# Kernel tuning notes

Hardware: AMD Instinct MI355X
Metric: run time of the kernel (lower is better)

Reference implementation:

```python
import jax, jax.numpy as jnp
import numpy as np

B, M, RPI = 16, 80, 256            # images, objects/image, relations/image
N, R = B * M, B * RPI
DF, REP, EMB, HID, NH, L = 12544, 1024, 256, 512, 8, 4
OBJC, RELC = 151, 51
IMW, IMH = 800.0, 600.0


def _ln(x, g, b):
    m = x.mean(-1, keepdims=True)
    v = ((x - m) ** 2).mean(-1, keepdims=True)
    return (x - m) * jax.lax.rsqrt(v + 1e-5) * g + b


def _encoder(x, qkv_w, qkv_b, out_w, out_b, f1_w, f1_b, f2_w, f2_b, ln1_s, ln1_b, ln2_s, ln2_b):
    # post-LN transformer encoder, L layers, x: [B, M, HID]
    Bb, Mm, D = x.shape
    dk = D // NH
    scale = 1.0 / jnp.sqrt(jnp.float32(dk))
    for l in range(L):
        qkv = x @ qkv_w[l].T + qkv_b[l]
        q, k, v = jnp.split(qkv, 3, axis=-1)
        hs = lambda t: t.reshape(Bb, Mm, NH, dk).transpose(0, 2, 1, 3)
        q, k, v = hs(q), hs(k), hs(v)
        att = jax.nn.softmax(jnp.einsum('bhqd,bhkd->bhqk', q, k) * scale, axis=-1)
        o = jnp.einsum('bhqk,bhkd->bhqd', att, v).transpose(0, 2, 1, 3).reshape(Bb, Mm, D)
        x = _ln(x + o @ out_w[l].T + out_b[l], ln1_s[l], ln1_b[l])
        f = jax.nn.relu(x @ f1_w[l].T + f1_b[l]) @ f2_w[l].T + f2_b[l]
        x = _ln(x + f, ln2_s[l], ln2_b[l])
    return x


def _box_info(boxes):
    wh = boxes[:, 2:] - boxes[:, :2] + 1.0
    xy = boxes[:, :2] + 0.5 * wh
    w, h = wh[:, :1], wh[:, 1:]
    x, y = xy[:, :1], xy[:, 1:]
    x1, y1, x2, y2 = boxes[:, 0:1], boxes[:, 1:2], boxes[:, 2:3], boxes[:, 3:4]
    return jnp.concatenate([w / IMW, h / IMH, x / IMW, y / IMH, x1 / IMW, y1 / IMH,
                            x2 / IMW, y2 / IMH, w * h / (IMW * IMH)], axis=-1)  # [N, 9]


def setup_inputs() -> dict:
    key = jax.random.key(0)
    ks = iter(jax.random.split(key, 80))
    nrm = lambda shape, s=0.02: jax.random.normal(next(ks), shape, jnp.float32) * s
    d = {}
    d['features'] = jax.random.normal(next(ks), (N, DF), jnp.float32)
    d['union_features'] = jax.random.normal(next(ks), (R, REP), jnp.float32)
    x1 = jax.random.uniform(next(ks), (N, 1)) * (IMW - 120.0)
    y1 = jax.random.uniform(next(ks), (N, 1)) * (IMH - 120.0)
    w = jax.random.uniform(next(ks), (N, 1)) * 100.0 + 5.0
    h = jax.random.uniform(next(ks), (N, 1)) * 100.0 + 5.0
    d['boxes'] = jnp.concatenate([x1, y1, x1 + w, y1 + h], axis=-1)
    d['logits'] = jax.random.normal(next(ks), (N, OBJC), jnp.float32)
    d['labels'] = jax.random.randint(next(ks), (N,), 0, OBJC)
    d['rel_pair_idxs'] = jax.random.randint(next(ks), (B, RPI, 2), 0, M)
    # feature extractor
    d['fe1_w'] = nrm((REP, DF)); d['fe1_b'] = jnp.zeros((REP,))
    d['fe2_w'] = nrm((REP, REP)); d['fe2_b'] = jnp.zeros((REP,))
    # embeddings
    d['emb1'] = nrm((OBJC, EMB), 1.0)
    d['emb2'] = nrm((OBJC, EMB), 1.0)
    # bbox embed 9->32->128
    d['bb1_w'] = nrm((32, 9)); d['bb1_b'] = jnp.zeros((32,))
    d['bb2_w'] = nrm((128, 32)); d['bb2_b'] = jnp.zeros((128,))
    d['lobj_w'] = nrm((HID, REP + EMB + 128)); d['lobj_b'] = jnp.zeros((HID,))
    d['ledge_w'] = nrm((HID, EMB + HID)); d['ledge_b'] = jnp.zeros((HID,))
    for p in ('o', 'e'):
        d[p + 'qkv_w'] = nrm((L, 3 * HID, HID)); d[p + 'qkv_b'] = jnp.zeros((L, 3 * HID))
        d[p + 'out_w'] = nrm((L, HID, HID)); d[p + 'out_b'] = jnp.zeros((L, HID))
        d[p + 'f1_w'] = nrm((L, HID, HID)); d[p + 'f1_b'] = jnp.zeros((L, HID))
        d[p + 'f2_w'] = nrm((L, HID, HID)); d[p + 'f2_b'] = jnp.zeros((L, HID))
        d[p + 'ln1_s'] = jnp.ones((L, HID)); d[p + 'ln1_b'] = jnp.zeros((L, HID))
        d[p + 'ln2_s'] = jnp.ones((L, HID)); d[p + 'ln2_b'] = jnp.zeros((L, HID))
    d['pcat_w'] = nrm((REP, 2 * HID)); d['pcat_b'] = jnp.zeros((REP,))
    d['fuse_w'] = nrm((REP, REP + HID)); d['fuse_b'] = jnp.zeros((REP,))
    d['cpx_w'] = nrm((RELC, 2 * REP)); d['cpx_b'] = jnp.zeros((RELC,))
    d['dpath_w'] = nrm((RELC, REP)); d['dpath_b'] = jnp.zeros((RELC,))
    return d


def reference(features, union_features, boxes, logits,
              fe1_w, fe1_b, fe2_w, fe2_b, emb1, emb2,
              bb1_w, bb1_b, bb2_w, bb2_b, lobj_w, lobj_b, ledge_w, ledge_b,
              oqkv_w, oqkv_b, oout_w, oout_b, of1_w, of1_b, of2_w, of2_b,
              oln1_s, oln1_b, oln2_s, oln2_b,
              eqkv_w, eqkv_b, eout_w, eout_b, ef1_w, ef1_b, ef2_w, ef2_b,
              eln1_s, eln1_b, eln2_s, eln2_b,
              pcat_w, pcat_b, fuse_w, fuse_b, cpx_w, cpx_b, dpath_w, dpath_b,
              labels, rel_pair_idxs):
    # FeatureExtractor
    bf = jax.nn.relu(features @ fe1_w.T + fe1_b)
    bf = jax.nn.relu(bf @ fe2_w.T + fe2_b)                        # [N, REP]
    # bbox embedding (dropout = identity in eval)
    pos = jax.nn.relu(_box_info(boxes) @ bb1_w.T + bb1_b)
    pos = jax.nn.relu(pos @ bb2_w.T + bb2_b)                      # [N, 128]
    obj_rep = jnp.concatenate([bf, emb1[labels], pos], -1) @ lobj_w.T + lobj_b  # [N, HID]
    obj_emb = _encoder(obj_rep.reshape(B, M, HID), oqkv_w, oqkv_b, oout_w, oout_b,
                       of1_w, of1_b, of2_w, of2_b, oln1_s, oln1_b, oln2_s, oln2_b)  # [B, M, HID]
    edge_in = jnp.concatenate([obj_emb.reshape(N, HID), emb2[labels]], -1) @ ledge_w.T + ledge_b
    gctx = _encoder(edge_in.reshape(B, M, HID), eqkv_w, eqkv_b, eout_w, eout_b,
                    ef1_w, ef1_b, ef2_w, ef2_b, eln1_s, eln1_b, eln2_s, eln2_b).mean(axis=1)  # [B, HID]
    # pair gather per image
    head = jax.vmap(lambda e, i: e[i])(obj_emb, rel_pair_idxs[:, :, 0])  # [B, RPI, HID]
    tail = jax.vmap(lambda e, i: e[i])(obj_emb, rel_pair_idxs[:, :, 1])
    pair = jnp.concatenate([head, tail], -1).reshape(R, 2 * HID)
    local = pair @ pcat_w.T + pcat_b                               # [R, REP]
    gexp = jnp.repeat(gctx, RPI, axis=0)                           # [R, HID]
    sem = jax.nn.relu(jnp.concatenate([local, gexp], -1) @ fuse_w.T + fuse_b)
    final = jnp.concatenate([sem, union_features], -1)             # [R, 2*REP]
    rel_logits = final @ cpx_w.T + cpx_b + local @ dpath_w.T + dpath_b  # [R, RELC]
    return rel_logits
```

## Files before the change

kernel.cpp:

```cpp
#include <hip/hip_runtime.h>
#include <hip/hip_bf16.h>
#include <cstdint>

#define DEV_INLINE __device__ __forceinline__

using u16 = unsigned short;
typedef __attribute__((ext_vector_type(8))) short bf8_t;
typedef __attribute__((ext_vector_type(4))) float f32x4;

constexpr int cB = 16, cM = 80, cRPI = 256;
constexpr int cN = cB * cM;
constexpr int cR = cB * cRPI;
constexpr int cDF = 12544, cREP = 1024, cEMB = 256, cHID = 512, cNH = 8, cL = 4;
constexpr int cRELC = 51;

DEV_INLINE u16 f2bf(float x) { return __builtin_bit_cast(u16, __float2bfloat16(x)); }
DEV_INLINE float bf2f(u16 u) { return __bfloat162float(__builtin_bit_cast(__hip_bfloat16, u)); }

DEV_INLINE float wave_max(float v) {
#pragma unroll
  for (int o = 32; o; o >>= 1) v = fmaxf(v, __shfl_xor(v, o));
  return v;
}
DEV_INLINE float wave_sum(float v) {
#pragma unroll
  for (int o = 32; o; o >>= 1) v += __shfl_xor(v, o);
  return v;
}

DEV_INLINE void xcd_remap(int& bx, int& by) {
  const int gx = gridDim.x;
  const int nwg = gx * gridDim.y;
  const int id = blockIdx.x + gx * blockIdx.y;
  const int q = nwg >> 3, r = nwg & 7;
  const int x = id & 7, k = id >> 3;
  const int idp = (x < r) ? x * (q + 1) + k : r * (q + 1) + (x - r) * q + k;
  bx = idp % gx;
  by = idp / gx;
}

template <int BM, int BN, bool SPLIT>
__global__ __launch_bounds__(256) void gemm_h(
    const u16* __restrict__ A, int lda,
    const u16* __restrict__ Bw, int ldb,
    int Mr, int Nr, int Klen,
    float* __restrict__ outF, int ldc,
    u16* __restrict__ outH, int ldh,
    const float* __restrict__ bias,
    const float* __restrict__ res, int resld, int resmode,
    int relu)
{
  constexpr int MF = BM / 32, NF = BN / 32;
  __shared__ u16 As[2][BM * 32];
  __shared__ u16 Bs[2][BN * 32];
  const int tid = threadIdx.x;
  const int wid = tid >> 6, lane = tid & 63;
  const int l15 = lane & 15, l4 = lane >> 4;
  int bx, by;
  xcd_remap(bx, by);
  const int bm = by * BM, bn = bx * BN;
  const int wr = wid >> 1, wc = wid & 1;
  const int kbase = SPLIT ? blockIdx.z * Klen : 0;

  f32x4 acc[MF][NF] = {};

  constexpr int AISS = (BM * 4) / 256;
  constexpr int BISS = (BN * 4) / 256;

  auto stage = [&](int buf, int ks) {
    const int k0 = kbase + (ks << 5);
#pragma unroll
    for (int i = 0; i < AISS; ++i) {
      const int c = i * 256 + tid;
      const int row = c >> 2, seg = c & 3;
      const int sseg = seg ^ (row & 3);
      const u16* gp = A + (size_t)(bm + row) * lda + k0 + sseg * 8;
      __builtin_amdgcn_global_load_lds(
          (const __attribute__((address_space(1))) void*)gp,
          (__attribute__((address_space(3))) void*)((char*)As[buf] + (size_t)(i * 256 + wid * 64) * 16),
          16, 0, 0);
    }
#pragma unroll
    for (int i = 0; i < BISS; ++i) {
      const int c = i * 256 + tid;
      const int row = c >> 2, seg = c & 3;
      const int sseg = seg ^ (row & 3);
      int brow = bn + row; if (brow > Nr - 1) brow = Nr - 1;
      const u16* gp = Bw + (size_t)brow * ldb + k0 + sseg * 8;
      __builtin_amdgcn_global_load_lds(
          (const __attribute__((address_space(1))) void*)gp,
          (__attribute__((address_space(3))) void*)((char*)Bs[buf] + (size_t)(i * 256 + wid * 64) * 16),
          16, 0, 0);
    }
  };

  const int nk = Klen >> 5;
  stage(0, 0);
  __syncthreads();

  for (int ks = 0; ks < nk; ++ks) {
    const int cur = ks & 1;
    if (ks + 1 < nk) stage(cur ^ 1, ks + 1);

    bf8_t af[MF], bfr[NF];
#pragma unroll
    for (int m = 0; m < MF; ++m) {
      const int r = wr * (BM / 2) + m * 16 + l15;
      const int g = l4 ^ (r & 3);
      af[m] = *(const bf8_t*)&As[cur][r * 32 + g * 8];
    }
#pragma unroll
    for (int n = 0; n < NF; ++n) {
      const int r = wc * (BN / 2) + n * 16 + l15;
      const int g = l4 ^ (r & 3);
      bfr[n] = *(const bf8_t*)&Bs[cur][r * 32 + g * 8];
    }
#pragma unroll
    for (int m = 0; m < MF; ++m)
#pragma unroll
      for (int n = 0; n < NF; ++n)
        acc[m][n] = __builtin_amdgcn_mfma_f32_16x16x32_bf16(af[m], bfr[n], acc[m][n], 0, 0, 0);
    __syncthreads();
  }

  if (SPLIT) {
    float* po = outF + (size_t)blockIdx.z * Mr * ldc;
#pragma unroll
    for (int m = 0; m < MF; ++m)
#pragma unroll
      for (int n = 0; n < NF; ++n) {
        const int ccol = bn + wc * (BN / 2) + n * 16 + l15;
        if (ccol >= Nr) continue;
#pragma unroll
        for (int g = 0; g < 4; ++g) {
          const int r = bm + wr * (BM / 2) + m * 16 + l4 * 4 + g;
          po[(size_t)r * ldc + ccol] = acc[m][n][g];
        }
      }
  } else {
#pragma unroll
    for (int m = 0; m < MF; ++m)
#pragma unroll
      for (int n = 0; n < NF; ++n) {
        const int ccol = bn + wc * (BN / 2) + n * 16 + l15;
        if (ccol >= Nr) continue;
        const float bv = bias ? bias[ccol] : 0.f;
#pragma unroll
        for (int g = 0; g < 4; ++g) {
          const int r = bm + wr * (BM / 2) + m * 16 + l4 * 4 + g;
          float v = acc[m][n][g] + bv;
          if (resmode == 1) v += res[(size_t)r * resld + ccol];
          else if (resmode == 2) v += res[(size_t)(r >> 8) * resld + ccol];
          if (relu) v = fmaxf(v, 0.f);
          if (outF) outF[(size_t)r * ldc + ccol] = v;
          if (outH) outH[(size_t)r * ldh + ccol] = f2bf(v);
        }
      }
  }
}

template <int BM, int BN>
static void g16(hipStream_t s, const u16* A, int lda, const u16* W, int ldb,
                int M, int N, int K, float* outF, int ldc, u16* outH, int ldh,
                const float* bias, const float* res, int resld, int resmode, int relu) {
  dim3 g((N + BN - 1) / BN, M / BM);
  gemm_h<BM, BN, false><<<g, 256, 0, s>>>(A, lda, W, ldb, M, N, K, outF, ldc, outH, ldh,
                                          bias, res, resld, resmode, relu);
}

__global__ __launch_bounds__(256) void gemm_nt(
    const float* __restrict__ A, int lda,
    const float* __restrict__ Bw, int ldb,
    float* __restrict__ C, int ldc,
    const float* __restrict__ bias,
    int Mr, int Nr, int Kr, int flags)
{
  __shared__ float As[16][68];
  __shared__ float Bs[16][68];
  const int tid = threadIdx.x;
  const int tx = tid & 15, ty = tid >> 4;
  const int bm = blockIdx.y * 64, bn = blockIdx.x * 64;
  const int lr = tid >> 2;
  const int lk = (tid & 3) * 4;

  float acc[4][4];
#pragma unroll
  for (int i = 0; i < 4; ++i)
#pragma unroll
    for (int j = 0; j < 4; ++j) acc[i][j] = 0.f;

  for (int k0 = 0; k0 < Kr; k0 += 16) {
    const int ar = bm + lr, br = bn + lr;
#pragma unroll
    for (int j = 0; j < 4; ++j) {
      const int kk = k0 + lk + j;
      float va = 0.f, vb = 0.f;
      if (kk < Kr) {
        if (ar < Mr) va = A[(size_t)ar * lda + kk];
        if (br < Nr) vb = Bw[(size_t)br * ldb + kk];
      }
      As[lk + j][lr] = va;
      Bs[lk + j][lr] = vb;
    }
    __syncthreads();
#pragma unroll
    for (int kk = 0; kk < 16; ++kk) {
      const float a0 = As[kk][ty * 4 + 0], a1 = As[kk][ty * 4 + 1],
                  a2 = As[kk][ty * 4 + 2], a3 = As[kk][ty * 4 + 3];
      const float b0 = Bs[kk][tx * 4 + 0], b1 = Bs[kk][tx * 4 + 1],
                  b2 = Bs[kk][tx * 4 + 2], b3 = Bs[kk][tx * 4 + 3];
      acc[0][0] += a0 * b0; acc[0][1] += a0 * b1; acc[0][2] += a0 * b2; acc[0][3] += a0 * b3;
      acc[1][0] += a1 * b0; acc[1][1] += a1 * b1; acc[1][2] += a1 * b2; acc[1][3] += a1 * b3;
      acc[2][0] += a2 * b0; acc[2][1] += a2 * b1; acc[2][2] += a2 * b2; acc[2][3] += a2 * b3;
      acc[3][0] += a3 * b0; acc[3][1] += a3 * b1; acc[3][2] += a3 * b2; acc[3][3] += a3 * b3;
    }
    __syncthreads();
  }
#pragma unroll
  for (int i = 0; i < 4; ++i) {
    const int r = bm + ty * 4 + i;
    if (r >= Mr) continue;
#pragma unroll
    for (int j = 0; j < 4; ++j) {
      const int c = bn + tx * 4 + j;
      if (c >= Nr) continue;
      float v = acc[i][j];
      if (bias) v += bias[c];
      if (flags & 2) v = fmaxf(v, 0.f);
      C[(size_t)r * ldc + c] = v;
    }
  }
}

__global__ void conv_kernel(const float* __restrict__ s, u16* __restrict__ d, int n4) {
  const int i = blockIdx.x * 256 + threadIdx.x;
  if (i >= n4) return;
  const float4 v = ((const float4*)s)[i];
  ushort4 o;
  o.x = f2bf(v.x); o.y = f2bf(v.y); o.z = f2bf(v.z); o.w = f2bf(v.w);
  ((ushort4*)d)[i] = o;
}

__global__ void conv2d_kernel(const float* __restrict__ src, int slda,
                              u16* __restrict__ dst, int dld, int cols) {
  const int r = blockIdx.x;
  for (int c = threadIdx.x; c < cols; c += blockDim.x)
    dst[(size_t)r * dld + c] = f2bf(src[(size_t)r * slda + c]);
}

__global__ void addb_kernel(const float* a, const float* b, float* o, int n) {
  const int i = threadIdx.x;
  if (i < n) o[i] = a[i] + b[i];
}

__global__ void box_info_kernel(const float* __restrict__ boxes, float* __restrict__ bi) {
  const int i = blockIdx.x * blockDim.x + threadIdx.x;
  if (i >= cN) return;
  const float x1 = boxes[i * 4 + 0], y1 = boxes[i * 4 + 1];
  const float x2 = boxes[i * 4 + 2], y2 = boxes[i * 4 + 3];
  const float w = x2 - x1 + 1.f, h = y2 - y1 + 1.f;
  const float cx = x1 + 0.5f * w, cy = y1 + 0.5f * h;
  float* o = bi + (size_t)i * 9;
  o[0] = w / 800.f;  o[1] = h / 600.f;
  o[2] = cx / 800.f; o[3] = cy / 600.f;
  o[4] = x1 / 800.f; o[5] = y1 / 600.f;
  o[6] = x2 / 800.f; o[7] = y2 / 600.f;
  o[8] = (w * h) / (800.f * 600.f);
}

__global__ void gather_emb_h(const float* __restrict__ emb, const int* __restrict__ labels,
                             u16* __restrict__ dst, int dld) {
  const int i = blockIdx.x;
  const int l = labels[i];
  const float* s = emb + (size_t)l * cEMB;
  for (int c = threadIdx.x; c < cEMB; c += blockDim.x)
    dst[(size_t)i * dld + c] = f2bf(s[c]);
}

__global__ __launch_bounds__(256) void attn_kernel(const u16* __restrict__ qkv,
                                                   u16* __restrict__ o) {
  __shared__ float Ks[80][65];
  __shared__ float Vs[80][65];
  const int bh = blockIdx.x;
  const int b = bh >> 3, h = bh & 7;
  const int tid = threadIdx.x;
  const u16* base = qkv + (size_t)(b * cM) * 1536 + h * 64;

  for (int e = tid; e < 80 * 64; e += 256) {
    const int r = e >> 6, d = e & 63;
    Ks[r][d] = bf2f(base[(size_t)r * 1536 + 512 + d]);
    Vs[r][d] = bf2f(base[(size_t)r * 1536 + 1024 + d]);
  }
  __syncthreads();

  const int wave = tid >> 6, lane = tid & 63;
  const int r0 = blockIdx.y * 16;
  for (int r = r0 + wave; r < r0 + 16; r += 4) {
    const float qd = bf2f(base[(size_t)r * 1536 + lane]);
    const int c2 = 64 + lane;
    const int c2c = (c2 < 80) ? c2 : 0;
    float s0 = 0.f, s1 = 0.f;
#pragma unroll 8
    for (int d = 0; d < 64; ++d) {
      const float qv = __shfl(qd, d);
      s0 += qv * Ks[lane][d];
      s1 += qv * Ks[c2c][d];
    }
    s0 *= 0.125f;
    s1 = (c2 < 80) ? s1 * 0.125f : -1e30f;
    const float mx = wave_max(fmaxf(s0, s1));
    const float p0 = __expf(s0 - mx);
    const float p1 = (c2 < 80) ? __expf(s1 - mx) : 0.f;
    const float ssum = wave_sum(p0 + p1);

    float od = 0.f;
#pragma unroll 8
    for (int c = 0; c < 64; ++c) od += __shfl(p0, c) * Vs[c][lane];
#pragma unroll
    for (int c = 0; c < 16; ++c) od += __shfl(p1, c) * Vs[64 + c][lane];
    od /= ssum;
    o[(size_t)(b * cM + r) * cHID + h * 64 + lane] = f2bf(od);
  }
}

__global__ __launch_bounds__(256) void ln_kernel(
    const float* __restrict__ in, float* __restrict__ outF,
    u16* __restrict__ outH, int ldh,
    const float* __restrict__ g, const float* __restrict__ bta) {
  const int row = blockIdx.x * 4 + (threadIdx.x >> 6);
  const int lane = threadIdx.x & 63;
  const float* x = in + (size_t)row * cHID;
  float v[8];
  float s = 0.f;
#pragma unroll
  for (int i = 0; i < 8; ++i) { v[i] = x[lane + i * 64]; s += v[i]; }
  s = wave_sum(s);
  const float mean = s * (1.f / 512.f);
  float vs = 0.f;
#pragma unroll
  for (int i = 0; i < 8; ++i) { const float d = v[i] - mean; vs += d * d; }
  vs = wave_sum(vs);
  const float inv = rsqrtf(vs * (1.f / 512.f) + 1e-5f);
#pragma unroll
  for (int i = 0; i < 8; ++i) {
    const int c = lane + i * 64;
    const float y = (v[i] - mean) * inv * g[c] + bta[c];
    outF[(size_t)row * cHID + c] = y;
    outH[(size_t)row * ldh + c] = f2bf(y);
  }
}

__global__ void mean_kernel(const float* __restrict__ x, float* __restrict__ gctx) {
  const int b = blockIdx.x;
  const int c = threadIdx.x;
  float s = 0.f;
  for (int m = 0; m < cM; ++m) s += x[(size_t)(b * cM + m) * cHID + c];
  gctx[(size_t)b * cHID + c] = s * (1.f / 80.f);
}

__global__ void pair_gather_h(const u16* __restrict__ obj, int old, const int* __restrict__ idx,
                              u16* __restrict__ pair) {
  const int r = blockIdx.x;
  const int b = r >> 8, rr = r & 255;
  const int i0 = idx[(size_t)(b * cRPI + rr) * 2 + 0];
  const int i1 = idx[(size_t)(b * cRPI + rr) * 2 + 1];
  const u16* hsrc = obj + (size_t)(b * cM + i0) * old;
  const u16* tsrc = obj + (size_t)(b * cM + i1) * old;
  u16* p = pair + (size_t)r * 1024;
  for (int c = threadIdx.x; c < cHID; c += blockDim.x) {
    p[c] = hsrc[c];
    p[cHID + c] = tsrc[c];
  }
}

__global__ void reduce8_kernel(const float* __restrict__ p, const float* __restrict__ bias,
                               u16* __restrict__ outH) {
  const int idx = blockIdx.x * 256 + threadIdx.x;
  constexpr int total = cN * cREP;
  if (idx >= total) return;
  float v = bias[idx & 1023];
#pragma unroll
  for (int z = 0; z < 8; ++z) v += p[(size_t)z * total + idx];
  outH[idx] = f2bf(fmaxf(v, 0.f));
}

__global__ void freduce_kernel(const float* __restrict__ p, const float* __restrict__ biasc,
                               float* __restrict__ out) {
  const int idx = blockIdx.x * 256 + threadIdx.x;
  if (idx >= cR * cRELC) return;
  const int r = idx / cRELC, c = idx - r * cRELC;
  float v = biasc[c];
#pragma unroll
  for (int z = 0; z < 4; ++z) v += p[(size_t)z * cR * 64 + (size_t)r * 64 + c];
  out[idx] = v;
}

static void run_encoder(hipStream_t s, float* x, u16* xh, u16* qkvh, u16* attn_h,
                        float* res1, u16* f_h,
                        const u16* qkvw, const float* qkvb,
                        const u16* outw, const float* outb,
                        const u16* f1w, const float* f1b,
                        const u16* f2w, const float* f2b,
                        const float* ln1s, const float* ln1b,
                        const float* ln2s, const float* ln2b,
                        u16* last_bf, int last_ld) {
  for (int l = 0; l < cL; ++l) {
    g16<64, 64>(s, xh, 512, qkvw + (size_t)l * 1536 * 512, 512, cN, 1536, 512,
                nullptr, 0, qkvh, 1536, qkvb + l * 1536, nullptr, 0, 0, 0);
    attn_kernel<<<dim3(cB * cNH, 5), 256, 0, s>>>(qkvh, attn_h);
    g16<64, 64>(s, attn_h, 512, outw + (size_t)l * 512 * 512, 512, cN, 512, 512,
                res1, 512, nullptr, 0, outb + l * 512, x, 512, 1, 0);
    ln_kernel<<<cN / 4, 256, 0, s>>>(res1, x, xh, 512, ln1s + l * 512, ln1b + l * 512);
    g16<64, 64>(s, xh, 512, f1w + (size_t)l * 512 * 512, 512, cN, 512, 512,
                nullptr, 0, f_h, 512, f1b + l * 512, nullptr, 0, 0, 1);
    g16<64, 64>(s, f_h, 512, f2w + (size_t)l * 512 * 512, 512, cN, 512, 512,
                res1, 512, nullptr, 0, f2b + l * 512, x, 512, 1, 0);
    const bool last = (l == cL - 1);
    ln_kernel<<<cN / 4, 256, 0, s>>>(res1, x, last ? last_bf : xh, last ? last_ld : 512,
                                     ln2s + l * 512, ln2b + l * 512);
  }
}

constexpr size_t OFF_FEAT  = 0;
constexpr size_t OFF_FE1W  = 32112640;
constexpr size_t OFF_PART  = 57802752;
constexpr size_t P_END     = 99745792;
constexpr size_t OFF_PAIR  = 0;
constexpr size_t OFF_FINAL = 8388608;
constexpr size_t OFF_OBJIN = 33554432;
constexpr size_t OFF_QKVH  = 37158912;
constexpr size_t OFF_X     = 41091072;
constexpr size_t OFF_XH    = 43712512;
constexpr size_t OFF_ATTN  = 45023232;
constexpr size_t OFF_RES   = 46333952;
constexpr size_t OFF_FH    = 48955392;
constexpr size_t OFF_EDGE  = 50266112;

extern "C" void kernel_launch(void* const* d_in, const int* in_sizes, int n_in,
                              void* d_out, int out_size, void* d_ws, size_t ws_size,
                              hipStream_t stream) {
  (void)in_sizes; (void)n_in; (void)out_size; (void)ws_size;

  const float* features = (const float*)d_in[0];
  const float* unionf   = (const float*)d_in[1];
  const float* boxes    = (const float*)d_in[2];
  const int*   labels   = (const int*)d_in[4];
  const int*   relidx   = (const int*)d_in[5];
  const float* fe1_w = (const float*)d_in[6];
  const float* fe1_b = (const float*)d_in[7];
  const float* fe2_w = (const float*)d_in[8];
  const float* fe2_b = (const float*)d_in[9];
  const float* emb1  = (const float*)d_in[10];
  const float* emb2  = (const float*)d_in[11];
  const float* bb1_w = (const float*)d_in[12];
  const float* bb1_b = (const float*)d_in[13];
  const float* bb2_w = (const float*)d_in[14];
  const float* bb2_b = (const float*)d_in[15];
  const float* lobj_w = (const float*)d_in[16];
  const float* lobj_b = (const float*)d_in[17];
  const float* ledge_w = (const float*)d_in[18];
  const float* ledge_b = (const float*)d_in[19];
  const float* oqkv_w = (const float*)d_in[20];
  const float* oqkv_b = (const float*)d_in[21];
  const float* oout_w = (const float*)d_in[22];
  const float* oout_b = (const float*)d_in[23];
  const float* of1_w = (const float*)d_in[24];
  const float* of1_b = (const float*)d_in[25];
  const float* of2_w = (const float*)d_in[26];
  const float* of2_b = (const float*)d_in[27];
  const float* oln1_s = (const float*)d_in[28];
  const float* oln1_b = (const float*)d_in[29];
  const float* oln2_s = (const float*)d_in[30];
  const float* oln2_b = (const float*)d_in[31];
  const float* eqkv_w = (const float*)d_in[32];
  const float* eqkv_b = (const float*)d_in[33];
  const float* eout_w = (const float*)d_in[34];
  const float* eout_b = (const float*)d_in[35];
  const float* ef1_w = (const float*)d_in[36];
  const float* ef1_b = (const float*)d_in[37];
  const float* ef2_w = (const float*)d_in[38];
  const float* ef2_b = (const float*)d_in[39];
  const float* eln1_s = (const float*)d_in[40];
  const float* eln1_b = (const float*)d_in[41];
  const float* eln2_s = (const float*)d_in[42];
  const float* eln2_b = (const float*)d_in[43];
  const float* pcat_w = (const float*)d_in[44];
  const float* pcat_b = (const float*)d_in[45];
  const float* fuse_w = (const float*)d_in[46];
  const float* fuse_b = (const float*)d_in[47];
  const float* cpx_w  = (const float*)d_in[48];
  const float* cpx_b  = (const float*)d_in[49];
  const float* dpath_w = (const float*)d_in[50];
  const float* dpath_b = (const float*)d_in[51];

  char* wsb = (char*)d_ws;
  u16* feat_h  = (u16*)(wsb + OFF_FEAT);
  u16* fe1w_h  = (u16*)(wsb + OFF_FE1W);
  float* part  = (float*)(wsb + OFF_PART);
  u16* pair    = (u16*)(wsb + OFF_PAIR);
  u16* finalb  = (u16*)(wsb + OFF_FINAL);
  u16* obj_in  = (u16*)(wsb + OFF_OBJIN);
  u16* qkvh    = (u16*)(wsb + OFF_QKVH);
  float* x     = (float*)(wsb + OFF_X);
  u16* xh      = (u16*)(wsb + OFF_XH);
  u16* attn_h  = (u16*)(wsb + OFF_ATTN);
  float* res1  = (float*)(wsb + OFF_RES);
  u16* f_h     = (u16*)(wsb + OFF_FH);
  u16* edge_in = (u16*)(wsb + OFF_EDGE);

  size_t off = P_END;
  auto alloc = [&](size_t bytes) { char* p = wsb + off; off = (off + bytes + 255) & ~(size_t)255; return p; };
  u16* fe2w_h   = (u16*)alloc(2097152);
  u16* lobjw_h  = (u16*)alloc(1441792);
  u16* ledgew_h = (u16*)alloc(786432);
  u16* oqkvw_h  = (u16*)alloc(6291456);
  u16* ooutw_h  = (u16*)alloc(2097152);
  u16* of1w_h   = (u16*)alloc(2097152);
  u16* of2w_h   = (u16*)alloc(2097152);
  u16* eqkvw_h  = (u16*)alloc(6291456);
  u16* eoutw_h  = (u16*)alloc(2097152);
  u16* ef1w_h   = (u16*)alloc(2097152);
  u16* ef2w_h   = (u16*)alloc(2097152);
  u16* pcatw_h  = (u16*)alloc(2097152);
  u16* fusew_h  = (u16*)alloc(3145728);
  u16* catw     = (u16*)alloc(313344);
  float* biasc  = (float*)alloc(256);
  u16* bf0h     = (u16*)alloc(2621440);
  float* gctx   = (float*)alloc(131072);
  u16* gctx_h   = (u16*)alloc(65536);
  float* gcproj = (float*)alloc(262144);
  float* binfo  = (float*)alloc(46080);
  float* pos1   = (float*)alloc(163840);
  float* pos2   = (float*)alloc(655360);
  float* fpart  = (float*)alloc(4194304);

  auto conv = [&](const float* s, u16* d, size_t n) {
    const int n4 = (int)(n / 4);
    conv_kernel<<<(n4 + 255) / 256, 256, 0, stream>>>(s, d, n4);
  };

  conv(features, feat_h, (size_t)cN * cDF);
  conv(fe1_w, fe1w_h, (size_t)cREP * cDF);
  conv(fe2_w, fe2w_h, (size_t)cREP * cREP);
  conv(lobj_w, lobjw_h, (size_t)cHID * 1408);
  conv(ledge_w, ledgew_h, (size_t)cHID * 768);
  conv(oqkv_w, oqkvw_h, (size_t)cL * 1536 * 512);
  conv(oout_w, ooutw_h, (size_t)cL * 512 * 512);
  conv(of1_w, of1w_h, (size_t)cL * 512 * 512);
  conv(of2_w, of2w_h, (size_t)cL * 512 * 512);
  conv(eqkv_w, eqkvw_h, (size_t)cL * 1536 * 512);
  conv(eout_w, eoutw_h, (size_t)cL * 512 * 512);
  conv(ef1_w, ef1w_h, (size_t)cL * 512 * 512);
  conv(ef2_w, ef2w_h, (size_t)cL * 512 * 512);
  conv(pcat_w, pcatw_h, (size_t)cREP * 1024);
  conv(fuse_w, fusew_h, (size_t)cREP * 1536);
  conv2d_kernel<<<cRELC, 256, 0, stream>>>(cpx_w, 2048, catw, 3072, 2048);
  conv2d_kernel<<<cRELC, 256, 0, stream>>>(dpath_w, 1024, catw + 2048, 3072, 1024);
  addb_kernel<<<1, 64, 0, stream>>>(cpx_b, dpath_b, biasc, cRELC);

  gemm_h<128, 128, true><<<dim3(8, 10, 8), 256, 0, stream>>>(
      feat_h, cDF, fe1w_h, cDF, cN, cREP, cDF / 8, part, cREP,
      nullptr, 0, nullptr, nullptr, 0, 0, 0);
  reduce8_kernel<<<(cN * cREP + 255) / 256, 256, 0, stream>>>(part, fe1_b, bf0h);

  box_info_kernel<<<(cN + 255) / 256, 256, 0, stream>>>(boxes, binfo);
  gemm_nt<<<dim3(1, 20), 256, 0, stream>>>(binfo, 9, bb1_w, 9, pos1, 32, bb1_b, cN, 32, 9, 2);
  gemm_nt<<<dim3(2, 20), 256, 0, stream>>>(pos1, 32, bb2_w, 32, pos2, 128, bb2_b, cN, 128, 32, 2);
  conv2d_kernel<<<cN, 128, 0, stream>>>(pos2, 128, obj_in + 1280, 1408, 128);
  gather_emb_h<<<cN, 256, 0, stream>>>(emb1, labels, obj_in + 1024, 1408);

  g16<64, 64>(stream, bf0h, 1024, fe2w_h, 1024, cN, cREP, cREP,
              nullptr, 0, obj_in, 1408, fe2_b, nullptr, 0, 0, 1);

  g16<64, 64>(stream, obj_in, 1408, lobjw_h, 1408, cN, cHID, 1408,
              x, 512, xh, 512, lobj_b, nullptr, 0, 0, 0);

  run_encoder(stream, x, xh, qkvh, attn_h, res1, f_h,
              oqkvw_h, oqkv_b, ooutw_h, oout_b, of1w_h, of1_b, of2w_h, of2_b,
              oln1_s, oln1_b, oln2_s, oln2_b, edge_in, 768);

  gather_emb_h<<<cN, 256, 0, stream>>>(emb2, labels, edge_in + 512, 768);
  pair_gather_h<<<cR, 256, 0, stream>>>(edge_in, 768, relidx, pair);

  g16<64, 64>(stream, edge_in, 768, ledgew_h, 768, cN, cHID, 768,
              x, 512, xh, 512, ledge_b, nullptr, 0, 0, 0);
  run_encoder(stream, x, xh, qkvh, attn_h, res1, f_h,
              eqkvw_h, eqkv_b, eoutw_h, eout_b, ef1w_h, ef1_b, ef2w_h, ef2_b,
              eln1_s, eln1_b, eln2_s, eln2_b, xh, 512);
  mean_kernel<<<cB, cHID, 0, stream>>>(x, gctx);

  conv2d_kernel<<<16, 256, 0, stream>>>(gctx, 512, gctx_h, 512, 512);
  g16<64, 64>(stream, gctx_h, 512, fusew_h + 1024, 1536, 64, cREP, 512,
              gcproj, 1024, nullptr, 0, fuse_b, nullptr, 0, 0, 0);

  conv2d_kernel<<<cR, 256, 0, stream>>>(unionf, 1024, finalb + 1024, 3072, 1024);
  g16<128, 64>(stream, pair, 1024, pcatw_h, 1024, cR, cREP, 1024,
               nullptr, 0, finalb + 2048, 3072, pcat_b, nullptr, 0, 0, 0);
  g16<128, 64>(stream, finalb + 2048, 3072, fusew_h, 1536, cR, cREP, 1024,
               nullptr, 0, finalb, 3072, nullptr, gcproj, 1024, 2, 1);

  gemm_h<64, 64, true><<<dim3(1, 64, 4), 256, 0, stream>>>(
      finalb, 3072, catw, 3072, cR, cRELC, 3072 / 4, fpart, 64,
      nullptr, 0, nullptr, nullptr, 0, 0, 0);
  freduce_kernel<<<(cR * cRELC + 255) / 256, 256, 0, stream>>>(fpart, biasc, (float*)d_out);
}
```

Baseline: 1.008 ms.

## Fuse LayerNorm into encoder GEMMs, batch conversions, merge box MLP prep

Adds a GEMM kernel that applies LayerNorm to the residual rows, stages the normalized bf16 row block in LDS, and then runs the QKV or FFN1 projection on it. This removes separate ln_kernel launches and round trips inside the encoder loop. It also merges the many per-weight fp32→bf16 conversion launches into a few grid-stride kernels, fuses the box-info, two small MLP layers and embedding gather into one prep kernel, and shrinks most GEMM tiles to 32x64 to get more blocks. The trade-off is that each column block recomputes the LayerNorm for its rows, and the smaller tiles give less data reuse per block.

```diff
diff --git a/kernel.cpp b/kernel.cpp
--- a/kernel.cpp
+++ b/kernel.cpp
@@ -50,7 +50,8 @@
     const float* __restrict__ res, int resld, int resmode,
     int relu)
 {
-  constexpr int MF = BM / 32, NF = BN / 32;
+  constexpr int MF = BM > 32 ? BM / 32 : 1, NF = BN > 32 ? BN / 32 : 1;
+  constexpr int ACH = BM * 4, BCH = BN * 4;
   __shared__ u16 As[2][BM * 32];
   __shared__ u16 Bs[2][BN * 32];
   const int tid = threadIdx.x;
@@ -64,33 +65,34 @@
 
   f32x4 acc[MF][NF] = {};
 
-  constexpr int AISS = (BM * 4) / 256;
-  constexpr int BISS = (BN * 4) / 256;
-
   auto stage = [&](int buf, int ks) {
     const int k0 = kbase + (ks << 5);
 #pragma unroll
-    for (int i = 0; i < AISS; ++i) {
+    for (int i = 0; i < (ACH + 255) / 256; ++i) {
       const int c = i * 256 + tid;
-      const int row = c >> 2, seg = c & 3;
-      const int sseg = seg ^ (row & 3);
-      const u16* gp = A + (size_t)(bm + row) * lda + k0 + sseg * 8;
-      __builtin_amdgcn_global_load_lds(
-          (const __attribute__((address_space(1))) void*)gp,
-          (__attribute__((address_space(3))) void*)((char*)As[buf] + (size_t)(i * 256 + wid * 64) * 16),
-          16, 0, 0);
-    }
-#pragma unroll
-    for (int i = 0; i < BISS; ++i) {
+      if (ACH % 256 == 0 || c < ACH) {
+        const int row = c >> 2, seg = c & 3;
+        const int sseg = seg ^ (row & 3);
+        const u16* gp = A + (size_t)(bm + row) * lda + k0 + sseg * 8;
+        __builtin_amdgcn_global_load_lds(
+            (const __attribute__((address_space(1))) void*)gp,
+            (__attribute__((address_space(3))) void*)((char*)As[buf] + (size_t)(i * 256 + wid * 64) * 16),
+            16, 0, 0);
+      }
+    }
+#pragma unroll
+    for (int i = 0; i < (BCH + 255) / 256; ++i) {
       const int c = i * 256 + tid;
-      const int row = c >> 2, seg = c & 3;
-      const int sseg = seg ^ (row & 3);
-      int brow = bn + row; if (brow > Nr - 1) brow = Nr - 1;
-      const u16* gp = Bw + (size_t)brow * ldb + k0 + sseg * 8;
-      __builtin_amdgcn_global_load_lds(
-          (const __attribute__((address_space(1))) void*)gp,
-          (__attribute__((address_space(3))) void*)((char*)Bs[buf] + (size_t)(i * 256 + wid * 64) * 16),
-          16, 0, 0);
+      if (BCH % 256 == 0 || c < BCH) {
+        const int row = c >> 2, seg = c & 3;
+        const int sseg = seg ^ (row & 3);
+        int brow = bn + row; if (brow > Nr - 1) brow = Nr - 1;
+        const u16* gp = Bw + (size_t)brow * ldb + k0 + sseg * 8;
+        __builtin_amdgcn_global_load_lds(
+            (const __attribute__((address_space(1))) void*)gp,
+            (__attribute__((address_space(3))) void*)((char*)Bs[buf] + (size_t)(i * 256 + wid * 64) * 16),
+            16, 0, 0);
+      }
     }
   };
 
@@ -168,77 +170,182 @@
                                           bias, res, resld, resmode, relu);
 }
 
-__global__ __launch_bounds__(256) void gemm_nt(
-    const float* __restrict__ A, int lda,
-    const float* __restrict__ Bw, int ldb,
-    float* __restrict__ C, int ldc,
-    const float* __restrict__ bias,
-    int Mr, int Nr, int Kr, int flags)
+__global__ __launch_bounds__(256) void gemm_lnA(
+    const float* __restrict__ res,
+    const float* __restrict__ lnS, const float* __restrict__ lnB,
+    const u16* __restrict__ W, int Nr,
+    u16* __restrict__ outH, int ldh,
+    const float* __restrict__ bias, int relu,
+    float* __restrict__ xout)
 {
-  __shared__ float As[16][68];
-  __shared__ float Bs[16][68];
+  __shared__ u16 As[32 * 512];
+  __shared__ u16 Bs[2][64 * 32];
   const int tid = threadIdx.x;
-  const int tx = tid & 15, ty = tid >> 4;
-  const int bm = blockIdx.y * 64, bn = blockIdx.x * 64;
-  const int lr = tid >> 2;
-  const int lk = (tid & 3) * 4;
-
-  float acc[4][4];
-#pragma unroll
-  for (int i = 0; i < 4; ++i)
-#pragma unroll
-    for (int j = 0; j < 4; ++j) acc[i][j] = 0.f;
-
-  for (int k0 = 0; k0 < Kr; k0 += 16) {
-    const int ar = bm + lr, br = bn + lr;
-#pragma unroll
-    for (int j = 0; j < 4; ++j) {
-      const int kk = k0 + lk + j;
-      float va = 0.f, vb = 0.f;
-      if (kk < Kr) {
-        if (ar < Mr) va = A[(size_t)ar * lda + kk];
-        if (br < Nr) vb = Bw[(size_t)br * ldb + kk];
-      }
-      As[lk + j][lr] = va;
-      Bs[lk + j][lr] = vb;
+  const int wid = tid >> 6, lane = tid & 63;
+  const int l15 = lane & 15, l4 = lane >> 4;
+  int bx, by;
+  xcd_remap(bx, by);
+  const int bm = by * 32, bn = bx * 64;
+  const int wr = wid >> 1, wc = wid & 1;
+
+  const int r8 = tid >> 3, sub = tid & 7;
+  const float4* rp4 = (const float4*)(res + (size_t)(bm + r8) * 512 + sub * 64);
+  float s = 0.f, q = 0.f;
+#pragma unroll
+  for (int k = 0; k < 16; ++k) {
+    const float4 v = rp4[k];
+    s += v.x + v.y + v.z + v.w;
+    q += v.x * v.x + v.y * v.y + v.z * v.z + v.w * v.w;
+  }
+#pragma unroll
+  for (int m = 1; m < 8; m <<= 1) { s += __shfl_xor(s, m); q += __shfl_xor(q, m); }
+  const float mean = s * (1.f / 512.f);
+  const float inv = rsqrtf(q * (1.f / 512.f) - mean * mean + 1e-5f);
+  const float4* ls4 = (const float4*)(lnS + sub * 64);
+  const float4* lb4 = (const float4*)(lnB + sub * 64);
+  float4* xo4 = (xout && bx == 0)
+      ? (float4*)(xout + (size_t)(bm + r8) * 512 + sub * 64) : nullptr;
+#pragma unroll
+  for (int k2 = 0; k2 < 8; ++k2) {
+    const float4 a = rp4[k2 * 2], b = rp4[k2 * 2 + 1];
+    const float4 sa = ls4[k2 * 2], sb = ls4[k2 * 2 + 1];
+    const float4 ba = lb4[k2 * 2], bb = lb4[k2 * 2 + 1];
+    float y0 = (a.x - mean) * inv * sa.x + ba.x;
+    float y1 = (a.y - mean) * inv * sa.y + ba.y;
+    float y2 = (a.z - mean) * inv * sa.z + ba.z;
+    float y3 = (a.w - mean) * inv * sa.w + ba.w;
+    float y4 = (b.x - mean) * inv * sb.x + bb.x;
+    float y5 = (b.y - mean) * inv * sb.y + bb.y;
+    float y6 = (b.z - mean) * inv * sb.z + bb.z;
+    float y7 = (b.w - mean) * inv * sb.w + bb.w;
+    bf8_t wv;
+    wv[0] = (short)f2bf(y0); wv[1] = (short)f2bf(y1);
+    wv[2] = (short)f2bf(y2); wv[3] = (short)f2bf(y3);
+    wv[4] = (short)f2bf(y4); wv[5] = (short)f2bf(y5);
+    wv[6] = (short)f2bf(y6); wv[7] = (short)f2bf(y7);
+    const int gsw = ((sub << 3) | k2) ^ (r8 & 7);
+    *(bf8_t*)&As[r8 * 512 + gsw * 8] = wv;
+    if (xo4) {
+      xo4[k2 * 2] = make_float4(y0, y1, y2, y3);
+      xo4[k2 * 2 + 1] = make_float4(y4, y5, y6, y7);
+    }
+  }
+
+  auto stageW = [&](int buf, int ks) {
+    const int row = tid >> 2, seg = tid & 3;
+    const int sseg = seg ^ (row & 3);
+    int brow = bn + row; if (brow > Nr - 1) brow = Nr - 1;
+    const u16* gp = W + (size_t)brow * 512 + (ks << 5) + sseg * 8;
+    __builtin_amdgcn_global_load_lds(
+        (const __attribute__((address_space(1))) void*)gp,
+        (__attribute__((address_space(3))) void*)((char*)Bs[buf] + (size_t)(wid * 64) * 16),
+        16, 0, 0);
+  };
+
+  stageW(0, 0);
+  __syncthreads();
+
+  f32x4 acc[2] = {};
+  for (int ks = 0; ks < 16; ++ks) {
+    const int cur = ks & 1;
+    if (ks + 1 < 16) stageW(cur ^ 1, ks + 1);
+
+    const int ra = wr * 16 + l15;
+    const int ga = ((ks << 2) | l4) ^ (ra & 7);
+    const bf8_t af = *(const bf8_t*)&As[ra * 512 + ga * 8];
+#pragma unroll
+    for (int n = 0; n < 2; ++n) {
+      const int rb = wc * 32 + n * 16 + l15;
+      const int gb = l4 ^ (rb & 3);
+      const bf8_t bv = *(const bf8_t*)&Bs[cur][rb * 32 + gb * 8];
+      acc[n] = __builtin_amdgcn_mfma_f32_16x16x32_bf16(af, bv, acc[n], 0, 0, 0);
     }
     __syncthreads();
-#pragma unroll
-    for (int kk = 0; kk < 16; ++kk) {
-      const float a0 = As[kk][ty * 4 + 0], a1 = As[kk][ty * 4 + 1],
-                  a2 = As[kk][ty * 4 + 2], a3 = As[kk][ty * 4 + 3];
-      const float b0 = Bs[kk][tx * 4 + 0], b1 = Bs[kk][tx * 4 + 1],
-                  b2 = Bs[kk][tx * 4 + 2], b3 = Bs[kk][tx * 4 + 3];
-      acc[0][0] += a0 * b0; acc[0][1] += a0 * b1; acc[0][2] += a0 * b2; acc[0][3] += a0 * b3;
-      acc[1][0] += a1 * b0; acc[1][1] += a1 * b1; acc[1][2] += a1 * b2; acc[1][3] += a1 * b3;
-      acc[2][0] += a2 * b0; acc[2][1] += a2 * b1; acc[2][2] += a2 * b2; acc[2][3] += a2 * b3;
-      acc[3][0] += a3 * b0; acc[3][1] += a3 * b1; acc[3][2] += a3 * b2; acc[3][3] += a3 * b3;
-    }
-    __syncthreads();
-  }
-#pragma unroll
-  for (int i = 0; i < 4; ++i) {
-    const int r = bm + ty * 4 + i;
-    if (r >= Mr) continue;
-#pragma unroll
-    for (int j = 0; j < 4; ++j) {
-      const int c = bn + tx * 4 + j;
-      if (c >= Nr) continue;
-      float v = acc[i][j];
-      if (bias) v += bias[c];
-      if (flags & 2) v = fmaxf(v, 0.f);
-      C[(size_t)r * ldc + c] = v;
-    }
-  }
-}
-
-__global__ void conv_kernel(const float* __restrict__ s, u16* __restrict__ d, int n4) {
-  const int i = blockIdx.x * 256 + threadIdx.x;
-  if (i >= n4) return;
-  const float4 v = ((const float4*)s)[i];
-  ushort4 o;
-  o.x = f2bf(v.x); o.y = f2bf(v.y); o.z = f2bf(v.z); o.w = f2bf(v.w);
-  ((ushort4*)d)[i] = o;
+  }
+
+#pragma unroll
+  for (int n = 0; n < 2; ++n) {
+    const int col = bn + wc * 32 + n * 16 + l15;
+    if (col >= Nr) continue;
+    const float bv = bias[col];
+#pragma unroll
+    for (int g = 0; g < 4; ++g) {
+      const int r = bm + wr * 16 + l4 * 4 + g;
+      float v = acc[n][g] + bv;
+      if (relu) v = fmaxf(v, 0.f);
+      outH[(size_t)r * ldh + col] = f2bf(v);
+    }
+  }
+}
+
+__global__ void conv_big2(const float* __restrict__ f, const float* __restrict__ w,
+                          u16* __restrict__ fh, u16* __restrict__ wh) {
+  constexpr int N1 = cN * cDF / 4;
+  constexpr int N2 = cREP * cDF / 4;
+  for (int i = blockIdx.x * 256 + threadIdx.x; i < N1 + N2; i += gridDim.x * 256) {
+    const float4 v = (i < N1) ? ((const float4*)f)[i] : ((const float4*)w)[i - N1];
+    ushort4 o = {f2bf(v.x), f2bf(v.y), f2bf(v.z), f2bf(v.w)};
+    if (i < N1) ((ushort4*)fh)[i] = o; else ((ushort4*)wh)[i - N1] = o;
+  }
+}
+
+constexpr size_t W_FE2 = 0, W_LOBJ = W_FE2 + 1048576, W_LEDGE = W_LOBJ + 720896,
+  W_OQKV = W_LEDGE + 393216, W_OOUT = W_OQKV + 3145728, W_OF1 = W_OOUT + 1048576,
+  W_OF2 = W_OF1 + 1048576, W_EQKV = W_OF2 + 1048576, W_EOUT = W_EQKV + 3145728,
+  W_EF1 = W_EOUT + 1048576, W_EF2 = W_EF1 + 1048576, W_PCAT = W_EF2 + 1048576,
+  W_FUSE = W_PCAT + 1048576, W_WEND = W_FUSE + 1572864;
+
+struct EncSrcs {
+  const float *fe2, *lobj, *ledge, *oqkv, *oout, *of1, *of2,
+              *eqkv, *eout, *ef1, *ef2, *pcat, *fuse;
+};
+
+__global__ void conv_enc(EncSrcs S, u16* __restrict__ wb) {
+#define SEG(nm, OFF, PRE, LEN) \
+  if (i < (PRE) + (LEN)) { \
+    const float4 v = ((const float4*)S.nm)[i - (PRE)]; \
+    ushort4 o = {f2bf(v.x), f2bf(v.y), f2bf(v.z), f2bf(v.w)}; \
+    ((ushort4*)(wb + (OFF)))[i - (PRE)] = o; \
+  } else
+  for (int i = blockIdx.x * 256 + threadIdx.x; i < (int)(W_WEND / 4); i += gridDim.x * 256) {
+    SEG(fe2,  W_FE2,   0,       262144)
+    SEG(lobj, W_LOBJ,  262144,  180224)
+    SEG(ledge,W_LEDGE, 442368,  98304)
+    SEG(oqkv, W_OQKV,  540672,  786432)
+    SEG(oout, W_OOUT,  1327104, 262144)
+    SEG(of1,  W_OF1,   1589248, 262144)
+    SEG(of2,  W_OF2,   1851392, 262144)
+    SEG(eqkv, W_EQKV,  2113536, 786432)
+    SEG(eout, W_EOUT,  2899968, 262144)
+    SEG(ef1,  W_EF1,   3162112, 262144)
+    SEG(ef2,  W_EF2,   3424256, 262144)
+    SEG(pcat, W_PCAT,  3686400, 262144)
+    SEG(fuse, W_FUSE,  3948544, 393216)
+    { }
+  }
+#undef SEG
+}
+
+__global__ void conv_cat(const float* __restrict__ cpx, const float* __restrict__ dpath,
+                         const float* __restrict__ cb, const float* __restrict__ db,
+                         u16* __restrict__ catw, float* __restrict__ biasc) {
+  constexpr int N1 = cRELC * 512;
+  constexpr int N2 = cRELC * 256;
+  const int i0 = blockIdx.x * 256 + threadIdx.x;
+  if (blockIdx.x == 0 && threadIdx.x < cRELC) biasc[threadIdx.x] = cb[threadIdx.x] + db[threadIdx.x];
+  for (int i = i0; i < N1 + N2; i += gridDim.x * 256) {
+    if (i < N1) {
+      const int r = i >> 9, c = i & 511;
+      const float4 v = ((const float4*)cpx)[i];
+      ushort4 o = {f2bf(v.x), f2bf(v.y), f2bf(v.z), f2bf(v.w)};
+      ((ushort4*)catw)[r * 768 + c] = o;
+    } else {
+      const int j = i - N1, r = j >> 8, c = j & 255;
+      const float4 v = ((const float4*)dpath)[j];
+      ushort4 o = {f2bf(v.x), f2bf(v.y), f2bf(v.z), f2bf(v.w)};
+      ((ushort4*)catw)[r * 768 + 512 + c] = o;
+    }
+  }
 }
 
 __global__ void conv2d_kernel(const float* __restrict__ src, int slda,
@@ -248,24 +355,43 @@
     dst[(size_t)r * dld + c] = f2bf(src[(size_t)r * slda + c]);
 }
 
-__global__ void addb_kernel(const float* a, const float* b, float* o, int n) {
-  const int i = threadIdx.x;
-  if (i < n) o[i] = a[i] + b[i];
-}
-
-__global__ void box_info_kernel(const float* __restrict__ boxes, float* __restrict__ bi) {
-  const int i = blockIdx.x * blockDim.x + threadIdx.x;
-  if (i >= cN) return;
-  const float x1 = boxes[i * 4 + 0], y1 = boxes[i * 4 + 1];
-  const float x2 = boxes[i * 4 + 2], y2 = boxes[i * 4 + 3];
+__global__ __launch_bounds__(256) void prep_obj(
+    const float* __restrict__ boxes,
+    const float* __restrict__ bb1w, const float* __restrict__ bb1b,
+    const float* __restrict__ bb2w, const float* __restrict__ bb2b,
+    const float* __restrict__ emb1, const int* __restrict__ labels,
+    u16* __restrict__ obj_in) {
+  __shared__ float W1[288];
+  __shared__ float W2[4096];
+  __shared__ float P1[8][33];
+  const int tid = threadIdx.x;
+  for (int i = tid; i < 288; i += 256) W1[i] = bb1w[i];
+  for (int i = tid; i < 4096; i += 256) W2[i] = bb2w[i];
+  __syncthreads();
+  const int r8 = tid >> 5, sub = tid & 31;
+  const int row = blockIdx.x * 8 + r8;
+  const float x1 = boxes[row * 4], y1 = boxes[row * 4 + 1];
+  const float x2 = boxes[row * 4 + 2], y2 = boxes[row * 4 + 3];
   const float w = x2 - x1 + 1.f, h = y2 - y1 + 1.f;
-  const float cx = x1 + 0.5f * w, cy = y1 + 0.5f * h;
-  float* o = bi + (size_t)i * 9;
-  o[0] = w / 800.f;  o[1] = h / 600.f;
-  o[2] = cx / 800.f; o[3] = cy / 600.f;
-  o[4] = x1 / 800.f; o[5] = y1 / 600.f;
-  o[6] = x2 / 800.f; o[7] = y2 / 600.f;
-  o[8] = (w * h) / (800.f * 600.f);
+  const float bi[9] = {w / 800.f, h / 600.f, (x1 + 0.5f * w) / 800.f, (y1 + 0.5f * h) / 600.f,
+                       x1 / 800.f, y1 / 600.f, x2 / 800.f, y2 / 600.f, w * h / 480000.f};
+  float p = bb1b[sub];
+#pragma unroll
+  for (int j = 0; j < 9; ++j) p += bi[j] * W1[sub * 9 + j];
+  P1[r8][sub] = fmaxf(p, 0.f);
+  __syncthreads();
+#pragma unroll
+  for (int jo = 0; jo < 4; ++jo) {
+    const int o = sub + jo * 32;
+    float a = bb2b[o];
+#pragma unroll
+    for (int j2 = 0; j2 < 32; ++j2) a += P1[r8][j2] * W2[o * 32 + j2];
+    obj_in[(size_t)row * 1408 + 1280 + o] = f2bf(fmaxf(a, 0.f));
+  }
+  const int l = labels[row];
+#pragma unroll
+  for (int k = 0; k < 8; ++k)
+    obj_in[(size_t)row * 1408 + 1024 + sub + k * 32] = f2bf(emb1[(size_t)l * 256 + sub + k * 32]);
 }
 
 __global__ void gather_emb_h(const float* __restrict__ emb, const int* __restrict__ labels,
@@ -350,12 +476,12 @@
   }
 }
 
-__global__ void mean_kernel(const float* __restrict__ x, float* __restrict__ gctx) {
+__global__ void mean_kernel(const float* __restrict__ x, u16* __restrict__ gctx_h) {
   const int b = blockIdx.x;
   const int c = threadIdx.x;
   float s = 0.f;
   for (int m = 0; m < cM; ++m) s += x[(size_t)(b * cM + m) * cHID + c];
-  gctx[(size_t)b * cHID + c] = s * (1.f / 80.f);
+  gctx_h[(size_t)b * cHID + c] = f2bf(s * (1.f / 80.f));
 }
 
 __global__ void pair_gather_h(const u16* __restrict__ obj, int old, const int* __restrict__ idx,
@@ -395,8 +521,8 @@
   out[idx] = v;
 }
 
-static void run_encoder(hipStream_t s, float* x, u16* xh, u16* qkvh, u16* attn_h,
-                        float* res1, u16* f_h,
+static void run_encoder(hipStream_t s, float* x, float* xa, float* res1,
+                        u16* xh, u16* qkvh, u16* attn_h, u16* f_h,
                         const u16* qkvw, const float* qkvb,
                         const u16* outw, const float* outb,
                         const u16* f1w, const float* f1b,
@@ -405,20 +531,26 @@
                         const float* ln2s, const float* ln2b,
                         u16* last_bf, int last_ld) {
   for (int l = 0; l < cL; ++l) {
-    g16<64, 64>(s, xh, 512, qkvw + (size_t)l * 1536 * 512, 512, cN, 1536, 512,
-                nullptr, 0, qkvh, 1536, qkvb + l * 1536, nullptr, 0, 0, 0);
+    if (l == 0) {
+      g16<32, 64>(s, xh, 512, qkvw, 512, cN, 1536, 512,
+                  nullptr, 0, qkvh, 1536, qkvb, nullptr, 0, 0, 0);
+    } else {
+      gemm_lnA<<<dim3(24, cN / 32), 256, 0, s>>>(
+          res1, ln2s + (l - 1) * 512, ln2b + (l - 1) * 512,
+          qkvw + (size_t)l * 1536 * 512, 1536, qkvh, 1536,
+          qkvb + l * 1536, 0, x);
+    }
     attn_kernel<<<dim3(cB * cNH, 5), 256, 0, s>>>(qkvh, attn_h);
-    g16<64, 64>(s, attn_h, 512, outw + (size_t)l * 512 * 512, 512, cN, 512, 512,
+    g16<32, 64>(s, attn_h, 512, outw + (size_t)l * 512 * 512, 512, cN, 512, 512,
                 res1, 512, nullptr, 0, outb + l * 512, x, 512, 1, 0);
-    ln_kernel<<<cN / 4, 256, 0, s>>>(res1, x, xh, 512, ln1s + l * 512, ln1b + l * 512);
-    g16<64, 64>(s, xh, 512, f1w + (size_t)l * 512 * 512, 512, cN, 512, 512,
-                nullptr, 0, f_h, 512, f1b + l * 512, nullptr, 0, 0, 1);
-    g16<64, 64>(s, f_h, 512, f2w + (size_t)l * 512 * 512, 512, cN, 512, 512,
-                res1, 512, nullptr, 0, f2b + l * 512, x, 512, 1, 0);
-    const bool last = (l == cL - 1);
-    ln_kernel<<<cN / 4, 256, 0, s>>>(res1, x, last ? last_bf : xh, last ? last_ld : 512,
-                                     ln2s + l * 512, ln2b + l * 512);
-  }
+    gemm_lnA<<<dim3(8, cN / 32), 256, 0, s>>>(
+        res1, ln1s + l * 512, ln1b + l * 512,
+        f1w + (size_t)l * 512 * 512, 512, f_h, 512, f1b + l * 512, 1, xa);
+    g16<32, 64>(s, f_h, 512, f2w + (size_t)l * 512 * 512, 512, cN, 512, 512,
+                res1, 512, nullptr, 0, f2b + l * 512, xa, 512, 1, 0);
+  }
+  ln_kernel<<<cN / 4, 256, 0, s>>>(res1, x, last_bf, last_ld,
+                                   ln2s + (cL - 1) * 512, ln2b + (cL - 1) * 512);
 }
 
 constexpr size_t OFF_FEAT  = 0;
@@ -435,6 +567,7 @@
 constexpr size_t OFF_RES   = 46333952;
 constexpr size_t OFF_FH    = 48955392;
 constexpr size_t OFF_EDGE  = 50266112;
+constexpr size_t OFF_XA    = 52232192;
 
 extern "C" void kernel_launch(void* const* d_in, const int* in_sizes, int n_in,
                               void* d_out, int out_size, void* d_ws, size_t ws_size,
@@ -507,90 +640,66 @@
   float* res1  = (float*)(wsb + OFF_RES);
   u16* f_h     = (u16*)(wsb + OFF_FH);
   u16* edge_in = (u16*)(wsb + OFF_EDGE);
+  float* xa    = (float*)(wsb + OFF_XA);
 
   size_t off = P_END;
   auto alloc = [&](size_t bytes) { char* p = wsb + off; off = (off + bytes + 255) & ~(size_t)255; return p; };
-  u16* fe2w_h   = (u16*)alloc(2097152);
-  u16* lobjw_h  = (u16*)alloc(1441792);
-  u16* ledgew_h = (u16*)alloc(786432);
-  u16* oqkvw_h  = (u16*)alloc(6291456);
-  u16* ooutw_h  = (u16*)alloc(2097152);
-  u16* of1w_h   = (u16*)alloc(2097152);
-  u16* of2w_h   = (u16*)alloc(2097152);
-  u16* eqkvw_h  = (u16*)alloc(6291456);
-  u16* eoutw_h  = (u16*)alloc(2097152);
-  u16* ef1w_h   = (u16*)alloc(2097152);
-  u16* ef2w_h   = (u16*)alloc(2097152);
-  u16* pcatw_h  = (u16*)alloc(2097152);
-  u16* fusew_h  = (u16*)alloc(3145728);
+  u16* wblock   = (u16*)alloc(W_WEND * 2);
   u16* catw     = (u16*)alloc(313344);
   float* biasc  = (float*)alloc(256);
   u16* bf0h     = (u16*)alloc(2621440);
-  float* gctx   = (float*)alloc(131072);
   u16* gctx_h   = (u16*)alloc(65536);
   float* gcproj = (float*)alloc(262144);
-  float* binfo  = (float*)alloc(46080);
-  float* pos1   = (float*)alloc(163840);
-  float* pos2   = (float*)alloc(655360);
   float* fpart  = (float*)alloc(4194304);
 
-  auto conv = [&](const float* s, u16* d, size_t n) {
-    const int n4 = (int)(n / 4);
-    conv_kernel<<<(n4 + 255) / 256, 256, 0, stream>>>(s, d, n4);
-  };
-
-  conv(features, feat_h, (size_t)cN * cDF);
-  conv(fe1_w, fe1w_h, (size_t)cREP * cDF);
-  conv(fe2_w, fe2w_h, (size_t)cREP * cREP);
-  conv(lobj_w, lobjw_h, (size_t)cHID * 1408);
-  conv(ledge_w, ledgew_h, (size_t)cHID * 768);
-  conv(oqkv_w, oqkvw_h, (size_t)cL * 1536 * 512);
-  conv(oout_w, ooutw_h, (size_t)cL * 512 * 512);
-  conv(of1_w, of1w_h, (size_t)cL * 512 * 512);
-  conv(of2_w, of2w_h, (size_t)cL * 512 * 512);
-  conv(eqkv_w, eqkvw_h, (size_t)cL * 1536 * 512);
-  conv(eout_w, eoutw_h, (size_t)cL * 512 * 512);
-  conv(ef1_w, ef1w_h, (size_t)cL * 512 * 512);
-  conv(ef2_w, ef2w_h, (size_t)cL * 512 * 512);
-  conv(pcat_w, pcatw_h, (size_t)cREP * 1024);
-  conv(fuse_w, fusew_h, (size_t)cREP * 1536);
-  conv2d_kernel<<<cRELC, 256, 0, stream>>>(cpx_w, 2048, catw, 3072, 2048);
-  conv2d_kernel<<<cRELC, 256, 0, stream>>>(dpath_w, 1024, catw + 2048, 3072, 1024);
-  addb_kernel<<<1, 64, 0, stream>>>(cpx_b, dpath_b, biasc, cRELC);
+  const u16* fe2w_h   = wblock + W_FE2;
+  const u16* lobjw_h  = wblock + W_LOBJ;
+  const u16* ledgew_h = wblock + W_LEDGE;
+  const u16* oqkvw_h  = wblock + W_OQKV;
+  const u16* ooutw_h  = wblock + W_OOUT;
+  const u16* of1w_h   = wblock + W_OF1;
+  const u16* of2w_h   = wblock + W_OF2;
+  const u16* eqkvw_h  = wblock + W_EQKV;
+  const u16* eoutw_h  = wblock + W_EOUT;
+  const u16* ef1w_h   = wblock + W_EF1;
+  const u16* ef2w_h   = wblock + W_EF2;
+  const u16* pcatw_h  = wblock + W_PCAT;
+  const u16* fusew_h  = wblock + W_FUSE;
+
+  conv_big2<<<2048, 256, 0, stream>>>(features, fe1_w, feat_h, fe1w_h);
+  EncSrcs es = {fe2_w, lobj_w, ledge_w, oqkv_w, oout_w, of1_w, of2_w,
+                eqkv_w, eout_w, ef1_w, ef2_w, pcat_w, fuse_w};
+  conv_enc<<<2048, 256, 0, stream>>>(es, wblock);
+  conv_cat<<<160, 256, 0, stream>>>(cpx_w, dpath_w, cpx_b, dpath_b, catw, biasc);
 
   gemm_h<128, 128, true><<<dim3(8, 10, 8), 256, 0, stream>>>(
       feat_h, cDF, fe1w_h, cDF, cN, cREP, cDF / 8, part, cREP,
       nullptr, 0, nullptr, nullptr, 0, 0, 0);
   reduce8_kernel<<<(cN * cREP + 255) / 256, 256, 0, stream>>>(part, fe1_b, bf0h);
 
-  box_info_kernel<<<(cN + 255) / 256, 256, 0, stream>>>(boxes, binfo);
-  gemm_nt<<<dim3(1, 20), 256, 0, stream>>>(binfo, 9, bb1_w, 9, pos1, 32, bb1_b, cN, 32, 9, 2);
-  gemm_nt<<<dim3(2, 20), 256, 0, stream>>>(pos1, 32, bb2_w, 32, pos2, 128, bb2_b, cN, 128, 32, 2);
-  conv2d_kernel<<<cN, 128, 0, stream>>>(pos2, 128, obj_in + 1280, 1408, 128);
-  gather_emb_h<<<cN, 256, 0, stream>>>(emb1, labels, obj_in + 1024, 1408);
-
-  g16<64, 64>(stream, bf0h, 1024, fe2w_h, 1024, cN, cREP, cREP,
+  prep_obj<<<cN / 8, 256, 0, stream>>>(boxes, bb1_w, bb1_b, bb2_w, bb2_b, emb1, labels, obj_in);
+
+  g16<32, 64>(stream, bf0h, 1024, fe2w_h, 1024, cN, cREP, cREP,
               nullptr, 0, obj_in, 1408, fe2_b, nullptr, 0, 0, 1);
 
-  g16<64, 64>(stream, obj_in, 1408, lobjw_h, 1408, cN, cHID, 1408,
+  g16<32, 64>(stream, obj_in, 1408, lobjw_h, 1408, cN, cHID, 1408,
               x, 512, xh, 512, lobj_b, nullptr, 0, 0, 0);
 
-  run_encoder(stream, x, xh, qkvh, attn_h, res1, f_h,
+  run_encoder(stream, x, xa, res1, xh, qkvh, attn_h, f_h,
               oqkvw_h, oqkv_b, ooutw_h, oout_b, of1w_h, of1_b, of2w_h, of2_b,
               oln1_s, oln1_b, oln2_s, oln2_b, edge_in, 768);
 
   gather_emb_h<<<cN, 256, 0, stream>>>(emb2, labels, edge_in + 512, 768);
   pair_gather_h<<<cR, 256, 0, stream>>>(edge_in, 768, relidx, pair);
 
-  g16<64, 64>(stream, edge_in, 768, ledgew_h, 768, cN, cHID, 768,
+  g16<32, 64>(stream, edge_in, 768, ledgew_h, 768, cN, cHID, 768,
               x, 512, xh, 512, ledge_b, nullptr, 0, 0, 0);
-  run_encoder(stream, x, xh, qkvh, attn_h, res1, f_h,
+  run_encoder(stream, x, xa, res1, xh, qkvh, attn_h, f_h,
               eqkvw_h, eqkv_b, eoutw_h, eout_b, ef1w_h, ef1_b, ef2w_h, ef2_b,
               eln1_s, eln1_b, eln2_s, eln2_b, xh, 512);
-  mean_kernel<<<cB, cHID, 0, stream>>>(x, gctx);
-
-  conv2d_kernel<<<16, 256, 0, stream>>>(gctx, 512, gctx_h, 512, 512);
-  g16<64, 64>(stream, gctx_h, 512, fusew_h + 1024, 1536, 64, cREP, 512,
+  mean_kernel<<<cB, cHID, 0, stream>>>(x, gctx_h);
+
+  g16<32, 64>(stream, gctx_h, 512, fusew_h + 1024, 1536, 64, cREP, 512,
               gcproj, 1024, nullptr, 0, fuse_b, nullptr, 0, 0, 0);
 
   conv2d_kernel<<<cR, 256, 0, stream>>>(unionf, 1024, finalb + 1024, 3072, 1024);
```

Result: slower. 1.153 ms (+14.3%).
